# Kernel tuning notes

Hardware: AMD Instinct MI355X
Metric: run time of the kernel (lower is better)

Reference implementation:

```python
import jax, jax.numpy as jnp
import numpy as np

M, D = 8192, 128
S_X, S_Y = 1.0, 1.0


def _gaussian_kernel(x, sigma):
    sq = jnp.sum(x * x, axis=-1)                      # [m]
    d2 = -2.0 * (x @ x.T) + sq[:, None] + sq[None, :]  # [m, m]
    return jnp.exp(-d2 / sigma)


def setup_inputs() -> dict:
    key = jax.random.key(0)
    kx, ky = jax.random.split(key)
    x = jax.random.normal(kx, (M, D), dtype=jnp.float32)
    y = jax.random.normal(ky, (M, D), dtype=jnp.float32)
    return {"x": x, "y": y}


def reference(x, y):
    m = x.shape[0]
    K = _gaussian_kernel(x, S_X)  # [m, m]
    L = _gaussian_kernel(y, S_Y)  # [m, m]
    # trace(L @ H @ K @ H) with H = I - (1/m) 11^T equals sum(L * center(K)),
    # where center(K) = K - row_mean - col_mean + total_mean (K, L symmetric).
    row_mean = jnp.mean(K, axis=1, keepdims=True)   # [m, 1]
    col_mean = jnp.mean(K, axis=0, keepdims=True)   # [1, m]
    tot_mean = jnp.mean(K)
    Kc = K - row_mean - col_mean + tot_mean
    hsic = jnp.sum(L * Kc) / jnp.asarray((m - 1) ** 2, dtype=x.dtype)
    return hsic
```

## Files before the change

kernel.cpp:

```cpp
#include <hip/hip_runtime.h>
#include <hip/hip_bf16.h>

typedef unsigned short u16;
typedef unsigned int   u32;

#define MM 8192
#define DD 128
#define NB 64
#define NTRI (NB * (NB + 1) / 2)
#define SKIP_THR -40.0f

using short8 = __attribute__((ext_vector_type(8))) short;
using f32x4  = __attribute__((ext_vector_type(4))) float;

__device__ __forceinline__ u16 f2bf(float f) {
  u32 u = __float_as_uint(f);
  u32 r = u + 0x7fffu + ((u >> 16) & 1u);
  return (u16)(r >> 16);
}

#define GLOAD_LDS16(g, l)                                          \
  __builtin_amdgcn_global_load_lds(                                \
      (const __attribute__((address_space(1))) void*)(g),          \
      (__attribute__((address_space(3))) void*)(l), 16, 0, 0)

__global__ __launch_bounds__(256) void convert_kernel(
    const float* __restrict__ x, const float* __restrict__ y,
    u16* __restrict__ xb, u16* __restrict__ yb,
    float* __restrict__ sqx, float* __restrict__ sqy)
{
  const int wid  = threadIdx.x >> 6;
  const int lane = threadIdx.x & 63;
  const int l32  = lane & 31;
  const int row  = blockIdx.x * 8 + wid * 2 + (lane >> 5);
  const float4 vx = *(const float4*)(x + (size_t)row * DD + l32 * 4);
  const float4 vy = *(const float4*)(y + (size_t)row * DD + l32 * 4);
  float sx = vx.x * vx.x + vx.y * vx.y + vx.z * vx.z + vx.w * vx.w;
  float sy = vy.x * vy.x + vy.y * vy.y + vy.z * vy.z + vy.w * vy.w;
  #pragma unroll
  for (int off = 1; off < 32; off <<= 1) {
    sx += __shfl_xor(sx, off, 64);
    sy += __shfl_xor(sy, off, 64);
  }
  uint2 px, py;
  px.x = (u32)f2bf(vx.x) | ((u32)f2bf(vx.y) << 16);
  px.y = (u32)f2bf(vx.z) | ((u32)f2bf(vx.w) << 16);
  py.x = (u32)f2bf(vy.x) | ((u32)f2bf(vy.y) << 16);
  py.y = (u32)f2bf(vy.z) | ((u32)f2bf(vy.w) << 16);
  *(uint2*)(xb + (size_t)row * DD + l32 * 4) = px;
  *(uint2*)(yb + (size_t)row * DD + l32 * 4) = py;
  if (l32 == 0) { sqx[row] = sx; sqy[row] = sy; }
}

__global__ __launch_bounds__(256, 2) void hsic_pair_kernel(
    const u16* __restrict__ xb, const u16* __restrict__ yb,
    const float* __restrict__ sqx, const float* __restrict__ sqy,
    float* __restrict__ comb_s, float* __restrict__ comb_t,
    float* __restrict__ P_part)
{
  const int bid = blockIdx.x;
  int ib = (int)(64.5f - sqrtf(64.5f * 64.5f - 2.0f * (float)bid));
  if (ib > NB - 1) ib = NB - 1;
  if (ib < 0) ib = 0;
  while (ib > 0 && (ib * NB - ib * (ib - 1) / 2) > bid) --ib;
  while (ib < NB - 1 && ((ib + 1) * NB - (ib + 1) * ib / 2) <= bid) ++ib;
  const int jb = ib + (bid - (ib * NB - ib * (ib - 1) / 2));

  const int i0   = ib * 128;
  const int j0   = jb * 128;
  const int tid  = threadIdx.x;
  const int wid  = tid >> 6;
  const int lane = tid & 63;
  const int wr   = wid >> 1;
  const int wc   = wid & 1;
  const int g    = lane >> 4;
  const int c    = lane & 15;

  const int ri = i0 + wr * 64;
  const int cj = j0 + wc * 64;

  __shared__ u16 lT[2][2][128 * 64];
  __shared__ float lds_sr[128], lds_sc[128], lds_tr[128], lds_tc[128];
  __shared__ float red[4];
  if (tid < 128) {
    lds_sr[tid] = 0.f; lds_sc[tid] = 0.f;
    lds_tr[tid] = 0.f; lds_tc[tid] = 0.f;
  }

  int so_[4];
  #pragma unroll
  for (int i = 0; i < 4; ++i) {
    const int o  = i * 4096 + tid * 16;
    const int r  = o >> 7;
    const int ch = (o >> 4) & 7;
    so_[i] = r * 256 + ((ch ^ (r & 7)) << 4);
  }

  const char* gAx = (const char*)xb + (size_t)i0 * 256;
  const char* gBx = (const char*)xb + (size_t)j0 * 256;
  const char* gAy = (const char*)yb + (size_t)i0 * 256;
  const char* gBy = (const char*)yb + (size_t)j0 * 256;

#define STAGE(R) do {                                                   \
    const char* gA_ = (((R) >> 1) ? gAy : gAx) + ((R) & 1) * 128;       \
    const char* gB_ = (((R) >> 1) ? gBy : gBx) + ((R) & 1) * 128;       \
    char* dA_ = (char*)&lT[(R) & 1][0][0] + wid * 1024;                 \
    char* dB_ = (char*)&lT[(R) & 1][1][0] + wid * 1024;                 \
    _Pragma("unroll") for (int i = 0; i < 4; ++i) {                     \
      GLOAD_LDS16(gA_ + so_[i], dA_ + i * 4096);                        \
      GLOAD_LDS16(gB_ + so_[i], dB_ + i * 4096);                        \
    }                                                                   \
  } while (0)

#define FRAG2(Lp, row, ch) \
  (*(const short8*)((Lp) + (((row) << 6) + (((ch) ^ ((row) & 7)) << 3))))

#define COMPUTE(ACC, BUF) do {                                          \
    _Pragma("unroll") for (int kk2 = 0; kk2 < 2; ++kk2) {               \
      short8 bfr[4], afr[4];                                            \
      _Pragma("unroll") for (int cs = 0; cs < 4; ++cs)                  \
        bfr[cs] = FRAG2(&lT[BUF][1][0], wc * 64 + cs * 16 + c, kk2 * 4 + g); \
      _Pragma("unroll") for (int rs = 0; rs < 4; ++rs)                  \
        afr[rs] = FRAG2(&lT[BUF][0][0], wr * 64 + rs * 16 + c, kk2 * 4 + g); \
      _Pragma("unroll") for (int rs = 0; rs < 4; ++rs)                  \
        _Pragma("unroll") for (int cs = 0; cs < 4; ++cs)                \
          ACC[rs][cs] = __builtin_amdgcn_mfma_f32_16x16x32_bf16(        \
              afr[rs], bfr[cs], ACC[rs][cs], 0, 0, 0);                  \
    }                                                                   \
  } while (0)

  f32x4 accX[4][4];
  f32x4 accY[4][4];
  #pragma unroll
  for (int rs = 0; rs < 4; ++rs)
    #pragma unroll
    for (int cs = 0; cs < 4; ++cs) {
      accX[rs][cs] = (f32x4){0.f, 0.f, 0.f, 0.f};
      accY[rs][cs] = (f32x4){0.f, 0.f, 0.f, 0.f};
    }

  STAGE(0);
  __syncthreads();
  STAGE(1); COMPUTE(accX, 0); __syncthreads();
  STAGE(2); COMPUTE(accX, 1); __syncthreads();
  STAGE(3); COMPUTE(accY, 0); __syncthreads();
            COMPUTE(accY, 1);

  float sqxc[4], sqyc[4];
  #pragma unroll
  for (int cs = 0; cs < 4; ++cs) {
    sqxc[cs] = sqx[cj + cs * 16 + c];
    sqyc[cs] = sqy[cj + cs * 16 + c];
  }

  float p_acc = 0.f;
  float scol_acc[4] = {0.f, 0.f, 0.f, 0.f};
  float tcol_acc[4] = {0.f, 0.f, 0.f, 0.f};

  #pragma unroll
  for (int rs = 0; rs < 4; ++rs) {
    const f32x4 sxr = *(const f32x4*)(sqx + ri + rs * 16 + g * 4);
    const f32x4 syr = *(const f32x4*)(sqy + ri + rs * 16 + g * 4);

    float sr_acc[4] = {0.f, 0.f, 0.f, 0.f};
    float tr_acc[4] = {0.f, 0.f, 0.f, 0.f};
    bool rowx = false, rowy = false;

    #pragma unroll
    for (int cs = 0; cs < 4; ++cs) {
      float ex[4], ey[4];
      #pragma unroll
      for (int tt = 0; tt < 4; ++tt) {
        ex[tt] = 2.f * accX[rs][cs][tt] - sxr[tt] - sqxc[cs];
        ey[tt] = 2.f * accY[rs][cs][tt] - syr[tt] - sqyc[cs];
      }
      const float mxx = fmaxf(fmaxf(ex[0], ex[1]), fmaxf(ex[2], ex[3]));
      const float mxy = fmaxf(fmaxf(ey[0], ey[1]), fmaxf(ey[2], ey[3]));
      const bool skipx = __all(mxx < SKIP_THR);
      const bool skipy = __all(mxy < SKIP_THR);
      if (skipx && skipy) continue;

      const int gc = cj + cs * 16 + c;
      float kx[4], ly[4];
      #pragma unroll
      for (int tt = 0; tt < 4; ++tt) {
        const int gr = ri + rs * 16 + g * 4 + tt;
        kx[tt] = skipx ? 0.f : ((gr == gc) ? 1.f : __expf(ex[tt]));
        ly[tt] = skipy ? 0.f : ((gr == gc) ? 1.f : __expf(ey[tt]));
      }
      if (!skipx) {
        rowx = true;
        float sc_ = 0.f;
        #pragma unroll
        for (int tt = 0; tt < 4; ++tt) { sr_acc[tt] += kx[tt]; sc_ += kx[tt]; }
        sc_ += __shfl_xor(sc_, 16, 64);
        sc_ += __shfl_xor(sc_, 32, 64);
        scol_acc[cs] += sc_;
      }
      if (!skipy) {
        rowy = true;
        float tc_ = 0.f;
        #pragma unroll
        for (int tt = 0; tt < 4; ++tt) { tr_acc[tt] += ly[tt]; tc_ += ly[tt]; }
        tc_ += __shfl_xor(tc_, 16, 64);
        tc_ += __shfl_xor(tc_, 32, 64);
        tcol_acc[cs] += tc_;
      }
      if (!skipx && !skipy) {
        #pragma unroll
        for (int tt = 0; tt < 4; ++tt) p_acc += kx[tt] * ly[tt];
      }
    }

    if (rowx) {
      #pragma unroll
      for (int tt = 0; tt < 4; ++tt) {
        float sv = sr_acc[tt];
        #pragma unroll
        for (int off = 1; off < 16; off <<= 1) sv += __shfl_xor(sv, off, 64);
        if (c == 0) atomicAdd(&lds_sr[wr * 64 + rs * 16 + g * 4 + tt], sv);
      }
    }
    if (rowy) {
      #pragma unroll
      for (int tt = 0; tt < 4; ++tt) {
        float tv = tr_acc[tt];
        #pragma unroll
        for (int off = 1; off < 16; off <<= 1) tv += __shfl_xor(tv, off, 64);
        if (c == 0) atomicAdd(&lds_tr[wr * 64 + rs * 16 + g * 4 + tt], tv);
      }
    }
  }

  if (g == 0) {
    #pragma unroll
    for (int cs = 0; cs < 4; ++cs) {
      atomicAdd(&lds_sc[wc * 64 + cs * 16 + c], scol_acc[cs]);
      atomicAdd(&lds_tc[wc * 64 + cs * 16 + c], tcol_acc[cs]);
    }
  }

  #pragma unroll
  for (int off = 1; off < 64; off <<= 1) p_acc += __shfl_xor(p_acc, off, 64);
  if (lane == 0) red[wid] = p_acc;
  __syncthreads();

  if (tid < 128) {
    comb_s[((size_t)ib * NB + jb) * 128 + tid] = lds_sr[tid];
    comb_t[((size_t)ib * NB + jb) * 128 + tid] = lds_tr[tid];
    if (ib != jb) {
      comb_s[((size_t)jb * NB + ib) * 128 + tid] = lds_sc[tid];
      comb_t[((size_t)jb * NB + ib) * 128 + tid] = lds_tc[tid];
    }
  }
  if (tid == 0) {
    const float w = (ib == jb) ? 1.f : 2.f;
    P_part[bid] = w * (red[0] + red[1] + red[2] + red[3]);
  }
}

__global__ __launch_bounds__(512) void reduce1_kernel(
    const float* __restrict__ comb_s, const float* __restrict__ comb_t,
    float* __restrict__ band_acc)
{
  const int b   = blockIdx.x;
  const int tid = threadIdx.x;
  const int row = tid & 127;
  const int grp = tid >> 7;

  float sv = 0.f, tv = 0.f;
  for (int k = grp * 16; k < grp * 16 + 16; ++k) {
    sv += comb_s[((size_t)b * NB + k) * 128 + row];
    tv += comb_t[((size_t)b * NB + k) * 128 + row];
  }
  __shared__ float ls[4][128], lt[4][128];
  ls[grp][row] = sv;
  lt[grp][row] = tv;
  __syncthreads();

  __shared__ float r2[2][3];
  if (tid < 128) {
    float S = ls[0][row] + ls[1][row] + ls[2][row] + ls[3][row];
    float T = lt[0][row] + lt[1][row] + lt[2][row] + lt[3][row];
    float C = S * T;
    #pragma unroll
    for (int off = 1; off < 64; off <<= 1) {
      S += __shfl_xor(S, off, 64);
      T += __shfl_xor(T, off, 64);
      C += __shfl_xor(C, off, 64);
    }
    if ((tid & 63) == 0) { r2[tid >> 6][0] = S; r2[tid >> 6][1] = T; r2[tid >> 6][2] = C; }
  }
  __syncthreads();
  if (tid == 0) {
    band_acc[b * 4 + 0] = r2[0][0] + r2[1][0];
    band_acc[b * 4 + 1] = r2[0][1] + r2[1][1];
    band_acc[b * 4 + 2] = r2[0][2] + r2[1][2];
  }
}

__global__ __launch_bounds__(256) void reduce2_kernel(
    const float* __restrict__ band_acc, const float* __restrict__ P_part,
    float* __restrict__ out)
{
  const int tid = threadIdx.x;
  float S = 0.f, T = 0.f, C = 0.f, P = 0.f;
  if (tid < NB) {
    S = band_acc[tid * 4 + 0];
    T = band_acc[tid * 4 + 1];
    C = band_acc[tid * 4 + 2];
  }
  for (int i = tid; i < NTRI; i += 256) P += P_part[i];
  #pragma unroll
  for (int off = 1; off < 64; off <<= 1) {
    S += __shfl_xor(S, off, 64);
    T += __shfl_xor(T, off, 64);
    C += __shfl_xor(C, off, 64);
    P += __shfl_xor(P, off, 64);
  }
  __shared__ float r[4][4];
  const int w = tid >> 6;
  if ((tid & 63) == 0) { r[w][0] = S; r[w][1] = T; r[w][2] = C; r[w][3] = P; }
  __syncthreads();
  if (tid == 0) {
    const double St = (double)r[0][0] + r[1][0] + r[2][0] + r[3][0];
    const double Tt = (double)r[0][1] + r[1][1] + r[2][1] + r[3][1];
    const double Ct = (double)r[0][2] + r[1][2] + r[2][2] + r[3][2];
    const double Pt = (double)r[0][3] + r[1][3] + r[2][3] + r[3][3];
    const double m  = (double)MM;
    const double num = Pt - (2.0 / m) * Ct + (St * Tt) / (m * m);
    out[0] = (float)(num / ((m - 1.0) * (m - 1.0)));
  }
}

extern "C" void kernel_launch(void* const* d_in, const int* in_sizes, int n_in,
                              void* d_out, int out_size, void* d_ws, size_t ws_size,
                              hipStream_t stream) {
  const float* x = (const float*)d_in[0];
  const float* y = (const float*)d_in[1];

  char* ws = (char*)d_ws;
  u16*   xb       = (u16*)ws;
  u16*   yb       = (u16*)(ws + (size_t)2 * 1024 * 1024);
  float* sqx      = (float*)(ws + (size_t)4 * 1024 * 1024);
  float* sqy      = sqx + MM;
  float* comb_s   = sqy + MM;
  float* comb_t   = comb_s + (size_t)NB * NB * 128;
  float* P_part   = comb_t + (size_t)NB * NB * 128;
  float* band_acc = P_part + NTRI;

  convert_kernel<<<MM / 8, 256, 0, stream>>>(x, y, xb, yb, sqx, sqy);

  hsic_pair_kernel<<<NTRI, 256, 0, stream>>>(xb, yb, sqx, sqy, comb_s, comb_t, P_part);

  reduce1_kernel<<<NB, 512, 0, stream>>>(comb_s, comb_t, band_acc);
  reduce2_kernel<<<1, 256, 0, stream>>>(band_acc, P_part, (float*)d_out);
}
```

Measured before the change: 61.10 us.

## Make pair kernel persistent with XCD-grouped tiles and cross-tile prefetch

Replaces the one-block-per-tile launch with 512 persistent blocks. Each block walks a strided list of tiles taken from a contiguous chunk of the triangular tile range assigned to its XCD. The first K-stage of the next tile is staged into LDS while the last MFMA stage of the current tile runs, and the LDS reduction buffers are re-zeroed between tiles. The goal is to cut block launch overhead, hide the initial load latency of each tile, and improve L2 reuse of shared row panels within an XCD. The cost is a static schedule that can leave some blocks with extra tiles, and more live state carried across loop iterations.

```diff
diff --git a/kernel.cpp b/kernel.cpp
--- a/kernel.cpp
+++ b/kernel.cpp
@@ -9,6 +9,8 @@
 #define NB 64
 #define NTRI (NB * (NB + 1) / 2)
 #define SKIP_THR -40.0f
+#define TPX 260
+#define BPX 64
 
 using short8 = __attribute__((ext_vector_type(8))) short;
 using f32x4  = __attribute__((ext_vector_type(4))) float;
@@ -52,22 +54,26 @@
   if (l32 == 0) { sqx[row] = sx; sqy[row] = sy; }
 }
 
+#define MAP(BID, IB, JB) do {                                           \
+    int ib_ = (int)(64.5f - sqrtf(64.5f * 64.5f - 2.0f * (float)(BID)));\
+    if (ib_ > NB - 1) ib_ = NB - 1;                                     \
+    if (ib_ < 0) ib_ = 0;                                               \
+    while (ib_ > 0 && (ib_ * NB - ib_ * (ib_ - 1) / 2) > (BID)) --ib_;  \
+    while (ib_ < NB - 1 && ((ib_ + 1) * NB - (ib_ + 1) * ib_ / 2) <= (BID)) ++ib_; \
+    (IB) = ib_;                                                         \
+    (JB) = ib_ + ((BID) - (ib_ * NB - ib_ * (ib_ - 1) / 2));            \
+  } while (0)
+
 __global__ __launch_bounds__(256, 2) void hsic_pair_kernel(
     const u16* __restrict__ xb, const u16* __restrict__ yb,
     const float* __restrict__ sqx, const float* __restrict__ sqy,
     float* __restrict__ comb_s, float* __restrict__ comb_t,
     float* __restrict__ P_part)
 {
-  const int bid = blockIdx.x;
-  int ib = (int)(64.5f - sqrtf(64.5f * 64.5f - 2.0f * (float)bid));
-  if (ib > NB - 1) ib = NB - 1;
-  if (ib < 0) ib = 0;
-  while (ib > 0 && (ib * NB - ib * (ib - 1) / 2) > bid) --ib;
-  while (ib < NB - 1 && ((ib + 1) * NB - (ib + 1) * ib / 2) <= bid) ++ib;
-  const int jb = ib + (bid - (ib * NB - ib * (ib - 1) / 2));
-
-  const int i0   = ib * 128;
-  const int j0   = jb * 128;
+  const int p   = blockIdx.x;
+  const int xcd = p & 7;
+  const int k0  = p >> 3;
+
   const int tid  = threadIdx.x;
   const int wid  = tid >> 6;
   const int lane = tid & 63;
@@ -76,9 +82,6 @@
   const int g    = lane >> 4;
   const int c    = lane & 15;
 
-  const int ri = i0 + wr * 64;
-  const int cj = j0 + wc * 64;
-
   __shared__ u16 lT[2][2][128 * 64];
   __shared__ float lds_sr[128], lds_sc[128], lds_tr[128], lds_tc[128];
   __shared__ float red[4];
@@ -96,16 +99,11 @@
     so_[i] = r * 256 + ((ch ^ (r & 7)) << 4);
   }
 
-  const char* gAx = (const char*)xb + (size_t)i0 * 256;
-  const char* gBx = (const char*)xb + (size_t)j0 * 256;
-  const char* gAy = (const char*)yb + (size_t)i0 * 256;
-  const char* gBy = (const char*)yb + (size_t)j0 * 256;
-
-#define STAGE(R) do {                                                   \
-    const char* gA_ = (((R) >> 1) ? gAy : gAx) + ((R) & 1) * 128;       \
-    const char* gB_ = (((R) >> 1) ? gBy : gBx) + ((R) & 1) * 128;       \
-    char* dA_ = (char*)&lT[(R) & 1][0][0] + wid * 1024;                 \
-    char* dB_ = (char*)&lT[(R) & 1][1][0] + wid * 1024;                 \
+#define STAGE(BUF, GA, GB, KH) do {                                     \
+    const char* gA_ = (GA) + (KH) * 128;                                \
+    const char* gB_ = (GB) + (KH) * 128;                                \
+    char* dA_ = (char*)&lT[BUF][0][0] + wid * 1024;                     \
+    char* dB_ = (char*)&lT[BUF][1][0] + wid * 1024;                     \
     _Pragma("unroll") for (int i = 0; i < 4; ++i) {                     \
       GLOAD_LDS16(gA_ + so_[i], dA_ + i * 4096);                        \
       GLOAD_LDS16(gB_ + so_[i], dB_ + i * 4096);                        \
@@ -129,133 +127,171 @@
     }                                                                   \
   } while (0)
 
-  f32x4 accX[4][4];
-  f32x4 accY[4][4];
-  #pragma unroll
-  for (int rs = 0; rs < 4; ++rs)
+  int k = k0;
+  int bid = xcd * TPX + k;
+  int ib, jb;
+  MAP(bid, ib, jb);
+  const char* gAx = (const char*)xb + (size_t)(ib * 128) * 256;
+  const char* gBx = (const char*)xb + (size_t)(jb * 128) * 256;
+  const char* gAy = (const char*)yb + (size_t)(ib * 128) * 256;
+  const char* gBy = (const char*)yb + (size_t)(jb * 128) * 256;
+
+  STAGE(0, gAx, gBx, 0);
+  __syncthreads();
+  int buf = 0;
+
+  while (true) {
+    f32x4 accX[4][4];
+    f32x4 accY[4][4];
+    #pragma unroll
+    for (int rs = 0; rs < 4; ++rs)
+      #pragma unroll
+      for (int cs = 0; cs < 4; ++cs) {
+        accX[rs][cs] = (f32x4){0.f, 0.f, 0.f, 0.f};
+        accY[rs][cs] = (f32x4){0.f, 0.f, 0.f, 0.f};
+      }
+
+    STAGE(buf ^ 1, gAx, gBx, 1);
+    COMPUTE(accX, buf); __syncthreads(); buf ^= 1;
+    STAGE(buf ^ 1, gAy, gBy, 0);
+    COMPUTE(accX, buf); __syncthreads(); buf ^= 1;
+    STAGE(buf ^ 1, gAy, gBy, 1);
+    COMPUTE(accY, buf); __syncthreads(); buf ^= 1;
+    const int kn = k + BPX;
+    const bool hasnext = (kn < TPX);
+    int nib = 0, njb = 0;
+    const char *nAx = 0, *nBx = 0, *nAy = 0, *nBy = 0;
+    if (hasnext) {
+      const int nbid = xcd * TPX + kn;
+      MAP(nbid, nib, njb);
+      nAx = (const char*)xb + (size_t)(nib * 128) * 256;
+      nBx = (const char*)xb + (size_t)(njb * 128) * 256;
+      nAy = (const char*)yb + (size_t)(nib * 128) * 256;
+      nBy = (const char*)yb + (size_t)(njb * 128) * 256;
+      STAGE(buf ^ 1, nAx, nBx, 0);
+    }
+    COMPUTE(accY, buf); __syncthreads(); buf ^= 1;
+
+    const int ri = ib * 128 + wr * 64;
+    const int cj = jb * 128 + wc * 64;
+
+    float sqxc[4], sqyc[4];
     #pragma unroll
     for (int cs = 0; cs < 4; ++cs) {
-      accX[rs][cs] = (f32x4){0.f, 0.f, 0.f, 0.f};
-      accY[rs][cs] = (f32x4){0.f, 0.f, 0.f, 0.f};
-    }
-
-  STAGE(0);
-  __syncthreads();
-  STAGE(1); COMPUTE(accX, 0); __syncthreads();
-  STAGE(2); COMPUTE(accX, 1); __syncthreads();
-  STAGE(3); COMPUTE(accY, 0); __syncthreads();
-            COMPUTE(accY, 1);
-
-  float sqxc[4], sqyc[4];
-  #pragma unroll
-  for (int cs = 0; cs < 4; ++cs) {
-    sqxc[cs] = sqx[cj + cs * 16 + c];
-    sqyc[cs] = sqy[cj + cs * 16 + c];
-  }
-
-  float p_acc = 0.f;
-  float scol_acc[4] = {0.f, 0.f, 0.f, 0.f};
-  float tcol_acc[4] = {0.f, 0.f, 0.f, 0.f};
-
-  #pragma unroll
-  for (int rs = 0; rs < 4; ++rs) {
-    const f32x4 sxr = *(const f32x4*)(sqx + ri + rs * 16 + g * 4);
-    const f32x4 syr = *(const f32x4*)(sqy + ri + rs * 16 + g * 4);
-
-    float sr_acc[4] = {0.f, 0.f, 0.f, 0.f};
-    float tr_acc[4] = {0.f, 0.f, 0.f, 0.f};
-    bool rowx = false, rowy = false;
-
-    #pragma unroll
-    for (int cs = 0; cs < 4; ++cs) {
-      float ex[4], ey[4];
+      sqxc[cs] = sqx[cj + cs * 16 + c];
+      sqyc[cs] = sqy[cj + cs * 16 + c];
+    }
+
+    float p_acc = 0.f;
+    float scol_acc[4] = {0.f, 0.f, 0.f, 0.f};
+    float tcol_acc[4] = {0.f, 0.f, 0.f, 0.f};
+
+    #pragma unroll
+    for (int rs = 0; rs < 4; ++rs) {
+      const f32x4 sxr = *(const f32x4*)(sqx + ri + rs * 16 + g * 4);
+      const f32x4 syr = *(const f32x4*)(sqy + ri + rs * 16 + g * 4);
+
+      float sr_acc[4] = {0.f, 0.f, 0.f, 0.f};
+      float tr_acc[4] = {0.f, 0.f, 0.f, 0.f};
+      bool rowx = false, rowy = false;
+
       #pragma unroll
-      for (int tt = 0; tt < 4; ++tt) {
-        ex[tt] = 2.f * accX[rs][cs][tt] - sxr[tt] - sqxc[cs];
-        ey[tt] = 2.f * accY[rs][cs][tt] - syr[tt] - sqyc[cs];
-      }
-      const float mxx = fmaxf(fmaxf(ex[0], ex[1]), fmaxf(ex[2], ex[3]));
-      const float mxy = fmaxf(fmaxf(ey[0], ey[1]), fmaxf(ey[2], ey[3]));
-      const bool skipx = __all(mxx < SKIP_THR);
-      const bool skipy = __all(mxy < SKIP_THR);
-      if (skipx && skipy) continue;
-
-      const int gc = cj + cs * 16 + c;
-      float kx[4], ly[4];
+      for (int cs = 0; cs < 4; ++cs) {
+        float ex[4], ey[4];
+        #pragma unroll
+        for (int tt = 0; tt < 4; ++tt) {
+          ex[tt] = 2.f * accX[rs][cs][tt] - sxr[tt] - sqxc[cs];
+          ey[tt] = 2.f * accY[rs][cs][tt] - syr[tt] - sqyc[cs];
+        }
+        const float mxx = fmaxf(fmaxf(ex[0], ex[1]), fmaxf(ex[2], ex[3]));
+        const float mxy = fmaxf(fmaxf(ey[0], ey[1]), fmaxf(ey[2], ey[3]));
+        const bool skipx = __all(mxx < SKIP_THR);
+        const bool skipy = __all(mxy < SKIP_THR);
+        if (skipx && skipy) continue;
+
+        const int gc = cj + cs * 16 + c;
+        float kx[4], ly[4];
+        #pragma unroll
+        for (int tt = 0; tt < 4; ++tt) {
+          const int gr = ri + rs * 16 + g * 4 + tt;
+          kx[tt] = skipx ? 0.f : ((gr == gc) ? 1.f : __expf(ex[tt]));
+          ly[tt] = skipy ? 0.f : ((gr == gc) ? 1.f : __expf(ey[tt]));
+        }
+        if (!skipx) {
+          rowx = true;
+          float sc_ = 0.f;
+          #pragma unroll
+          for (int tt = 0; tt < 4; ++tt) { sr_acc[tt] += kx[tt]; sc_ += kx[tt]; }
+          sc_ += __shfl_xor(sc_, 16, 64);
+          sc_ += __shfl_xor(sc_, 32, 64);
+          scol_acc[cs] += sc_;
+        }
+        if (!skipy) {
+          rowy = true;
+          float tc_ = 0.f;
+          #pragma unroll
+          for (int tt = 0; tt < 4; ++tt) { tr_acc[tt] += ly[tt]; tc_ += ly[tt]; }
+          tc_ += __shfl_xor(tc_, 16, 64);
+          tc_ += __shfl_xor(tc_, 32, 64);
+          tcol_acc[cs] += tc_;
+        }
+        if (!skipx && !skipy) {
+          #pragma unroll
+          for (int tt = 0; tt < 4; ++tt) p_acc += kx[tt] * ly[tt];
+        }
+      }
+
+      if (rowx) {
+        #pragma unroll
+        for (int tt = 0; tt < 4; ++tt) {
+          float sv = sr_acc[tt];
+          #pragma unroll
+          for (int off = 1; off < 16; off <<= 1) sv += __shfl_xor(sv, off, 64);
+          if (c == 0) atomicAdd(&lds_sr[wr * 64 + rs * 16 + g * 4 + tt], sv);
+        }
+      }
+      if (rowy) {
+        #pragma unroll
+        for (int tt = 0; tt < 4; ++tt) {
+          float tv = tr_acc[tt];
+          #pragma unroll
+          for (int off = 1; off < 16; off <<= 1) tv += __shfl_xor(tv, off, 64);
+          if (c == 0) atomicAdd(&lds_tr[wr * 64 + rs * 16 + g * 4 + tt], tv);
+        }
+      }
+    }
+
+    if (g == 0) {
       #pragma unroll
-      for (int tt = 0; tt < 4; ++tt) {
-        const int gr = ri + rs * 16 + g * 4 + tt;
-        kx[tt] = skipx ? 0.f : ((gr == gc) ? 1.f : __expf(ex[tt]));
-        ly[tt] = skipy ? 0.f : ((gr == gc) ? 1.f : __expf(ey[tt]));
-      }
-      if (!skipx) {
-        rowx = true;
-        float sc_ = 0.f;
-        #pragma unroll
-        for (int tt = 0; tt < 4; ++tt) { sr_acc[tt] += kx[tt]; sc_ += kx[tt]; }
-        sc_ += __shfl_xor(sc_, 16, 64);
-        sc_ += __shfl_xor(sc_, 32, 64);
-        scol_acc[cs] += sc_;
-      }
-      if (!skipy) {
-        rowy = true;
-        float tc_ = 0.f;
-        #pragma unroll
-        for (int tt = 0; tt < 4; ++tt) { tr_acc[tt] += ly[tt]; tc_ += ly[tt]; }
-        tc_ += __shfl_xor(tc_, 16, 64);
-        tc_ += __shfl_xor(tc_, 32, 64);
-        tcol_acc[cs] += tc_;
-      }
-      if (!skipx && !skipy) {
-        #pragma unroll
-        for (int tt = 0; tt < 4; ++tt) p_acc += kx[tt] * ly[tt];
-      }
-    }
-
-    if (rowx) {
-      #pragma unroll
-      for (int tt = 0; tt < 4; ++tt) {
-        float sv = sr_acc[tt];
-        #pragma unroll
-        for (int off = 1; off < 16; off <<= 1) sv += __shfl_xor(sv, off, 64);
-        if (c == 0) atomicAdd(&lds_sr[wr * 64 + rs * 16 + g * 4 + tt], sv);
-      }
-    }
-    if (rowy) {
-      #pragma unroll
-      for (int tt = 0; tt < 4; ++tt) {
-        float tv = tr_acc[tt];
-        #pragma unroll
-        for (int off = 1; off < 16; off <<= 1) tv += __shfl_xor(tv, off, 64);
-        if (c == 0) atomicAdd(&lds_tr[wr * 64 + rs * 16 + g * 4 + tt], tv);
-      }
-    }
-  }
-
-  if (g == 0) {
-    #pragma unroll
-    for (int cs = 0; cs < 4; ++cs) {
-      atomicAdd(&lds_sc[wc * 64 + cs * 16 + c], scol_acc[cs]);
-      atomicAdd(&lds_tc[wc * 64 + cs * 16 + c], tcol_acc[cs]);
-    }
-  }
-
-  #pragma unroll
-  for (int off = 1; off < 64; off <<= 1) p_acc += __shfl_xor(p_acc, off, 64);
-  if (lane == 0) red[wid] = p_acc;
-  __syncthreads();
-
-  if (tid < 128) {
-    comb_s[((size_t)ib * NB + jb) * 128 + tid] = lds_sr[tid];
-    comb_t[((size_t)ib * NB + jb) * 128 + tid] = lds_tr[tid];
-    if (ib != jb) {
-      comb_s[((size_t)jb * NB + ib) * 128 + tid] = lds_sc[tid];
-      comb_t[((size_t)jb * NB + ib) * 128 + tid] = lds_tc[tid];
-    }
-  }
-  if (tid == 0) {
-    const float w = (ib == jb) ? 1.f : 2.f;
-    P_part[bid] = w * (red[0] + red[1] + red[2] + red[3]);
+      for (int cs = 0; cs < 4; ++cs) {
+        atomicAdd(&lds_sc[wc * 64 + cs * 16 + c], scol_acc[cs]);
+        atomicAdd(&lds_tc[wc * 64 + cs * 16 + c], tcol_acc[cs]);
+      }
+    }
+
+    #pragma unroll
+    for (int off = 1; off < 64; off <<= 1) p_acc += __shfl_xor(p_acc, off, 64);
+    if (lane == 0) red[wid] = p_acc;
+    __syncthreads();
+
+    if (tid < 128) {
+      comb_s[((size_t)ib * NB + jb) * 128 + tid] = lds_sr[tid];
+      comb_t[((size_t)ib * NB + jb) * 128 + tid] = lds_tr[tid];
+      if (ib != jb) {
+        comb_s[((size_t)jb * NB + ib) * 128 + tid] = lds_sc[tid];
+        comb_t[((size_t)jb * NB + ib) * 128 + tid] = lds_tc[tid];
+      }
+      lds_sr[tid] = 0.f; lds_sc[tid] = 0.f;
+      lds_tr[tid] = 0.f; lds_tc[tid] = 0.f;
+    }
+    if (tid == 0) {
+      const float w = (ib == jb) ? 1.f : 2.f;
+      P_part[bid] = w * (red[0] + red[1] + red[2] + red[3]);
+    }
+
+    if (!hasnext) break;
+    k = kn; bid = xcd * TPX + kn; ib = nib; jb = njb;
+    gAx = nAx; gBx = nBx; gAy = nAy; gBy = nBy;
   }
 }
 
@@ -351,7 +387,7 @@
 
   convert_kernel<<<MM / 8, 256, 0, stream>>>(x, y, xb, yb, sqx, sqy);
 
-  hsic_pair_kernel<<<NTRI, 256, 0, stream>>>(xb, yb, sqx, sqy, comb_s, comb_t, P_part);
+  hsic_pair_kernel<<<512, 256, 0, stream>>>(xb, yb, sqx, sqy, comb_s, comb_t, P_part);
 
   reduce1_kernel<<<NB, 512, 0, stream>>>(comb_s, comb_t, band_acc);
   reduce2_kernel<<<1, 256, 0, stream>>>(band_acc, P_part, (float*)d_out);
```

Result: slower. 64.20 us (+5.1%).
